# Kernel tuning notes

Measured on AMD Instinct MI355X. Metric: run time of the kernel, lower is better.

## Reference

```python
import jax, jax.numpy as jnp
import numpy as np

NEG = -1e30  # safe 'log zero' for fp32 (avoids -inf NaNs in grads)


def _ctc_loss(logits, targets, input_lengths, target_lengths):
    """PyTorch-semantics CTC loss: blank=0, reduction='mean', zero_infinity=True.
    logits: [B,T,C] (pre-log-softmax), targets: [B,S] padded, lengths: [B].
    """
    B, T, C = logits.shape
    S = targets.shape[1]
    L = 2 * S + 1  # extended target length (blanks interleaved)
    logp = jax.nn.log_softmax(logits, axis=-1)  # [B,T,C]

    # extended targets: blank, y1, blank, y2, ..., blank
    ext = jnp.zeros((B, L), jnp.int32).at[:, 1::2].set(targets.astype(jnp.int32))
    lp_ext = jnp.take_along_axis(
        logp, jnp.broadcast_to(ext[:, None, :], (B, T, L)), axis=2)  # [B,T,L]

    pos = jnp.arange(L)
    ext_m2 = jnp.pad(ext, ((0, 0), (2, 0)))[:, :L]
    can_skip = (ext != 0) & (ext != ext_m2) & (pos >= 2)  # [B,L]

    def shift(a, k):
        return jnp.pad(a, ((0, 0), (k, 0)), constant_values=NEG)[:, :L]

    def lse3(a, b, c):
        m = jnp.maximum(jnp.maximum(a, b), c)
        return m + jnp.log(jnp.exp(a - m) + jnp.exp(b - m) + jnp.exp(c - m))

    alpha0 = (jnp.full((B, L), NEG, logits.dtype)
              .at[:, 0].set(lp_ext[:, 0, 0])
              .at[:, 1].set(lp_ext[:, 0, 1]))

    def step(alpha, xs):
        lp_t, t = xs  # lp_t: [B,L]
        a2 = shift(alpha, 1)
        a3 = jnp.where(can_skip, shift(alpha, 2), NEG)
        new = lp_t + lse3(alpha, a2, a3)
        # freeze alpha once past each sample's input_length
        alpha = jnp.where((t < input_lengths)[:, None], new, alpha)
        return alpha, None

    lp_T = jnp.swapaxes(lp_ext, 0, 1)  # [T,B,L]
    alpha, _ = jax.lax.scan(step, alpha0, (lp_T[1:], jnp.arange(1, T)))

    i1 = (2 * target_lengths - 1).astype(jnp.int32)
    i2 = (2 * target_lengths).astype(jnp.int32)
    a_last = jnp.take_along_axis(alpha, i1[:, None], axis=1)[:, 0]
    a_blank = jnp.take_along_axis(alpha, i2[:, None], axis=1)[:, 0]
    loss = -jnp.logaddexp(a_last, a_blank)  # [B]
    loss = jnp.where(loss > 1e29, 0.0, loss)  # zero_infinity=True
    return jnp.mean(loss / target_lengths.astype(loss.dtype))


def setup_inputs() -> dict:
    key = jax.random.key(0)
    ks = jax.random.split(key, 8)
    B, T = 32, 2000
    C_err, S_err = 4, 50
    C_ph, S_ph = 64, 200
    error_logits = jax.random.normal(ks[0], (B, T, C_err), jnp.float32)
    phoneme_logits = jax.random.normal(ks[1], (B, T, C_ph), jnp.float32)
    # labels in [1, C): blank=0 never appears in targets
    error_targets = jax.random.randint(ks[2], (B, S_err), 1, C_err, jnp.int32)
    phoneme_targets = jax.random.randint(ks[3], (B, S_ph), 1, C_ph, jnp.int32)
    error_input_lengths = jax.random.randint(ks[4], (B,), T - T // 4, T + 1, jnp.int32)
    phoneme_input_lengths = jax.random.randint(ks[5], (B,), T - T // 4, T + 1, jnp.int32)
    error_target_lengths = jax.random.randint(ks[6], (B,), S_err // 2, S_err + 1, jnp.int32)
    phoneme_target_lengths = jax.random.randint(ks[7], (B,), S_ph // 2, S_ph + 1, jnp.int32)
    return {
        "error_logits": error_logits,
        "phoneme_logits": phoneme_logits,
        "error_targets": error_targets,
        "phoneme_targets": phoneme_targets,
        "error_input_lengths": error_input_lengths,
        "phoneme_input_lengths": phoneme_input_lengths,
        "error_target_lengths": error_target_lengths,
        "phoneme_target_lengths": phoneme_target_lengths,
    }


def reference(error_logits, phoneme_logits, error_targets, phoneme_targets,
              error_input_lengths, phoneme_input_lengths,
              error_target_lengths, phoneme_target_lengths):
    error_weight = 1.0
    phoneme_weight = 1.0
    error_loss = _ctc_loss(error_logits, error_targets,
                           error_input_lengths, error_target_lengths)
    phoneme_loss = _ctc_loss(phoneme_logits, phoneme_targets,
                             phoneme_input_lengths, phoneme_target_lengths)
    total_loss = error_weight * error_loss + phoneme_weight * phoneme_loss
    return total_loss
```

## Files before the change

kernel.cpp:

```cpp
#include <hip/hip_runtime.h>
#include <math.h>


static constexpr float  LOG2E = 1.4426950408889634f;
static constexpr double LN2D  = 0.6931471805599453;
static constexpr int GROWS = 2032;

#define DPP_WAVE_SHR1   0x138
#define DPP_ROW_SHR(n)  (0x110 | (n))
#define DPP_ROW_BCAST15 0x142
#define DPP_ROW_BCAST31 0x143

__device__ __forceinline__ float fexp2(float x) {
  return __builtin_amdgcn_exp2f(x);
}
__device__ __forceinline__ float flog2(float x) {
  return __builtin_amdgcn_logf(x);
}

__device__ __forceinline__ double dpp_shr1_f64(double x) {
  int lo = __double2loint(x), hi = __double2hiint(x);
  lo = __builtin_amdgcn_update_dpp(0, lo, DPP_WAVE_SHR1, 0xf, 0xf, true);
  hi = __builtin_amdgcn_update_dpp(0, hi, DPP_WAVE_SHR1, 0xf, 0xf, true);
  return __hiloint2double(hi, lo);
}

__device__ __forceinline__ int imax2(int a, int b) { return a > b ? a : b; }

__device__ __forceinline__ int wave_imax(int v) {
  v = imax2(v, __builtin_amdgcn_update_dpp(0, v, DPP_ROW_SHR(1), 0xf, 0xf, true));
  v = imax2(v, __builtin_amdgcn_update_dpp(0, v, DPP_ROW_SHR(2), 0xf, 0xf, true));
  v = imax2(v, __builtin_amdgcn_update_dpp(0, v, DPP_ROW_SHR(4), 0xf, 0xf, true));
  v = imax2(v, __builtin_amdgcn_update_dpp(0, v, DPP_ROW_SHR(8), 0xf, 0xf, true));
  v = imax2(v, __builtin_amdgcn_update_dpp(0, v, DPP_ROW_BCAST15, 0xf, 0xf, true));
  v = imax2(v, __builtin_amdgcn_update_dpp(0, v, DPP_ROW_BCAST31, 0xf, 0xf, true));
  return __builtin_amdgcn_readlane(v, 63);
}

__device__ __forceinline__ void wait_lgkm0() {
  __builtin_amdgcn_sched_barrier(0);
  __builtin_amdgcn_s_waitcnt(49279);
  __builtin_amdgcn_sched_barrier(0);
}


__global__ __launch_bounds__(256) void gather_ph_kernel(
    const float* __restrict__ ph_logits, const float* __restrict__ err_logits,
    const int* __restrict__ ph_tgt,
    float* __restrict__ Gph, float* __restrict__ Lpb_ph,
    float* __restrict__ Lpb_er, float* __restrict__ out) {
  const int bx = blockIdx.x, b = blockIdx.y;
  const int tid = threadIdx.x;
  const int lane = tid & 63, wv = tid >> 6;

  if (bx == 0 && b == 0 && tid == 0) *out = 0.f;

  if (wv == 0 && lane < 32) {
    const int t = bx * 32 + lane;
    if (t < 2000) {
      const float4 v = *(const float4*)(err_logits + ((size_t)b * 2000 + t) * 4);
      const float z0 = v.x * LOG2E;
      const float s = fexp2(z0) + fexp2(v.y * LOG2E) + fexp2(v.z * LOG2E) +
                      fexp2(v.w * LOG2E);
      Lpb_er[(size_t)b * GROWS + t] = z0 - flog2(s);
    }
  }

  const int* tb = ph_tgt + b * 200;
  int idx[4];
  float msk[4];
#pragma unroll
  for (int k = 0; k < 4; ++k) {
    const int si = lane * 4 + k;
    const int cls = (si < 200) ? tb[si] : 0;
    idx[k] = cls << 2;
    msk[k] = (si < 200) ? 1.0f : 0.0f;
  }
  const int t0 = (bx * 4 + wv) * 8;
  float z[8], e[8], s[8];
#pragma unroll
  for (int u = 0; u < 8; ++u) {
    const int t = t0 + u;
    const int tc = (t < 2000) ? t : 1999;
    z[u] = ph_logits[((size_t)b * 2000 + tc) * 64 + lane] * LOG2E;
    e[u] = fexp2(z[u]);
    s[u] = e[u];
  }
#pragma unroll
  for (int off = 32; off >= 1; off >>= 1) {
#pragma unroll
    for (int u = 0; u < 8; ++u) s[u] += __shfl_xor(s[u], off, 64);
  }
#pragma unroll
  for (int u = 0; u < 8; ++u) {
    const int t = t0 + u;
    if (t < 2000) {
      const float e0 = __int_as_float(
          __builtin_amdgcn_readlane(__float_as_int(e[u]), 0));
      const float inv0 = 1.0f / e0;
      float o[4];
#pragma unroll
      for (int k = 0; k < 4; ++k) {
        const float v = __int_as_float(
            __builtin_amdgcn_ds_bpermute(idx[k], __float_as_int(e[u])));
        o[k] = msk[k] * v * inv0;
      }
      *(float4*)(Gph + ((size_t)b * GROWS + t) * 256 + lane * 4) =
          make_float4(o[0], o[1], o[2], o[3]);
      if (lane == 0)
        Lpb_ph[(size_t)b * GROWS + t] = z[u] - flog2(s[u]);
    }
  }
}

template <int P> struct RowP { float v[P]; };

__device__ __forceinline__ RowP<4> ld4(const float* p) {
  RowP<4> r;
  const float4 a = *(const float4*)p;
  r.v[0] = a.x; r.v[1] = a.y; r.v[2] = a.z; r.v[3] = a.w;
  return r;
}

template <int P>
__device__ __forceinline__ void bl_renorm(double (&B)[P], double (&L)[P],
                                          int& K) {
  double mm = B[0];
#pragma unroll
  for (int k = 0; k < P; ++k) mm = fmax(fmax(mm, B[k]), L[k]);
  const int ex = (__double2hiint(mm) >> 20) & 0x7ff;
  const int emax = wave_imax(ex);
  if (emax > 0) {
    int d = 1523 - emax;
    if (d > 1023) d = 1023;
    if (d < -1022) d = -1022;
    const double sc = __hiloint2double((d + 1023) << 20, 0);
#pragma unroll
    for (int k = 0; k < P; ++k) { B[k] *= sc; L[k] *= sc; }
    K += d;
  }
}

template <int P>
__device__ __forceinline__ void bl_step(double (&B)[P], double (&L)[P],
                                        const double (&skipm)[P],
                                        const RowP<P>& f) {
  const double Lm1 = dpp_shr1_f64(L[P - 1]);
  double nB[P], nL[P];
#pragma unroll
  for (int k = 0; k < P; ++k) {
    const double Lp = (k >= 1) ? L[k - 1] : Lm1;
    nB[k] = B[k] + Lp;
    nL[k] = (double)f.v[k] * fma(skipm[k], Lp, B[k] + L[k]);
  }
#pragma unroll
  for (int k = 0; k < P; ++k) { B[k] = nB[k]; L[k] = nL[k]; }
}

__device__ __forceinline__ float spb_sum(const float* __restrict__ Lpb,
                                         int len, int lane) {
  float spb = 0.f;
  for (int t0 = lane; t0 < len; t0 += 512) {
#pragma unroll
    for (int u = 0; u < 8; ++u) {
      const int t = t0 + u * 64;
      const int tc = (t < len) ? t : 0;
      const float v = Lpb[tc];
      spb += (t < len) ? v : 0.0f;
    }
  }
#pragma unroll
  for (int off = 32; off >= 1; off >>= 1) spb += __shfl_xor(spb, off, 64);
  return spb;
}

__global__ __launch_bounds__(64) void ctc_chains2_kernel(
    const float* __restrict__ Gph, const float* __restrict__ err_logits,
    const int* __restrict__ ph_tgt, const int* __restrict__ err_tgt,
    const int* __restrict__ err_il, const int* __restrict__ ph_il,
    const int* __restrict__ err_tl, const int* __restrict__ ph_tl,
    const float* __restrict__ Lpb_ph, const float* __restrict__ Lpb_er,
    float* __restrict__ out) {
  __shared__ double sa[512];
  const int blk = blockIdx.x;
  const int lane = threadIdx.x;

  if (blk < 32) {
    constexpr int S = 50;
    const int c = blk;
    const int* tb = err_tgt + c * 50;
    int len = err_il[c]; if (len > 2000) len = 2000;
    const int tl = err_tl[c];
    const float4* zr = (const float4*)(err_logits + (size_t)c * 2000 * 4);

    const float spb = spb_sum(Lpb_er + (size_t)c * GROWS, len, lane);
    const int c1 = tb[(lane < S) ? lane : (S - 1)];
    const float fmask = (lane < S) ? 1.0f : 0.0f;
    double skipm[1];
    skipm[0] = (lane >= 1 && lane < S && tb[lane] != tb[lane - 1]) ? 1.0 : 0.0;

    double B[1], L[1];
    B[0] = 0.0; L[0] = 0.0;
    {
      const float4 q0 = zr[0];
      const int c0 = tb[0];
      const float zc = (c0 == 1) ? q0.y : (c0 == 2) ? q0.z : q0.w;
      if (lane == 0) {
        B[0] = 1.0;
        L[0] = (double)fexp2((zc - q0.x) * LOG2E);
      }
    }
    int K = 0;

    const int nsteps = len - 1;
    const int ng = nsteps / 8;
    float4 bufA[8], bufB[8];
    if (ng >= 1) {
#pragma unroll
      for (int u = 0; u < 8; ++u) bufA[u] = zr[1 + u];
    }
    if (ng >= 2) {
#pragma unroll
      for (int u = 0; u < 8; ++u) bufB[u] = zr[9 + u];
    }
    int g = 0;
    for (; g + 2 <= ng; g += 2) {
      bl_renorm<1>(B, L, K);
      {
        const int gn = (g + 2 < ng) ? (g + 2) : 0;
        const float4* nx = zr + 1 + gn * 8;
#pragma unroll
        for (int u = 0; u < 8; ++u) {
          RowP<1> f;
          const float4 q = bufA[u];
          const float zc = (c1 == 1) ? q.y : (c1 == 2) ? q.z : q.w;
          f.v[0] = fmask * fexp2((zc - q.x) * LOG2E);
          bl_step<1>(B, L, skipm, f);
          bufA[u] = nx[u];
        }
      }
      bl_renorm<1>(B, L, K);
      {
        const int gn = (g + 3 < ng) ? (g + 3) : 0;
        const float4* nx = zr + 1 + gn * 8;
#pragma unroll
        for (int u = 0; u < 8; ++u) {
          RowP<1> f;
          const float4 q = bufB[u];
          const float zc = (c1 == 1) ? q.y : (c1 == 2) ? q.z : q.w;
          f.v[0] = fmask * fexp2((zc - q.x) * LOG2E);
          bl_step<1>(B, L, skipm, f);
          bufB[u] = nx[u];
        }
      }
    }
    if (g < ng) {
      bl_renorm<1>(B, L, K);
#pragma unroll
      for (int u = 0; u < 8; ++u) {
        RowP<1> f;
        const float4 q = bufA[u];
        const float zc = (c1 == 1) ? q.y : (c1 == 2) ? q.z : q.w;
        f.v[0] = fmask * fexp2((zc - q.x) * LOG2E);
        bl_step<1>(B, L, skipm, f);
      }
      ++g;
    }
    {
      const int tstart = 1 + ng * 8;
      float4 bufT[7];
#pragma unroll
      for (int u = 0; u < 7; ++u) {
        int t = tstart + u;
        if (t > nsteps) t = (nsteps > 0) ? nsteps : 1;
        bufT[u] = zr[t];
      }
#pragma unroll
      for (int u = 0; u < 7; ++u) {
        if (tstart + u <= nsteps) {
          if (u == 0) bl_renorm<1>(B, L, K);
          RowP<1> f;
          const float4 q = bufT[u];
          const float zc = (c1 == 1) ? q.y : (c1 == 2) ? q.z : q.w;
          f.v[0] = fmask * fexp2((zc - q.x) * LOG2E);
          bl_step<1>(B, L, skipm, f);
        }
      }
    }

    double* saB = sa;
    double* saL = sa + 64;
    saB[lane] = B[0];
    saL[lane] = L[0];
    wait_lgkm0();
    if (lane == 0) {
      const double a = saL[tl - 1] + saB[tl];
      float loss = (float)((double)K * LN2D - log(a) - (double)spb * LN2D);
      if (!(loss < 1e29f)) loss = 0.f;
      atomicAdd(out, loss / ((float)tl * 32.0f));
    }
    return;
  }

  constexpr int P = 4, S = 200, LSTRIDE = 256;
  const int b = blk - 32;
  const int* tb = ph_tgt + b * 200;
  int len = ph_il[b]; if (len > 2000) len = 2000;
  const int tl = ph_tl[b];
  const float* Glab = Gph + (size_t)b * GROWS * 256;
  const float* gp = Glab + lane * P;

  const float spb = spb_sum(Lpb_ph + (size_t)b * GROWS, len, lane);

  double skipm[P];
#pragma unroll
  for (int k = 0; k < P; ++k) {
    const int s = lane * P + k;
    skipm[k] = (s >= 1 && s < S && tb[s] != tb[s - 1]) ? 1.0 : 0.0;
  }

  double B[P], L[P];
#pragma unroll
  for (int k = 0; k < P; ++k) { B[k] = 0.0; L[k] = 0.0; }
  {
    const float r0 = Glab[0];
    if (lane == 0) { B[0] = 1.0; L[0] = (double)r0; }
  }
  int K = 0;

  const int ngroups = (len - 1) / 16;

  RowP<P> bufA[16], bufB[16];
  if (ngroups >= 1) {
    const float* rb = gp + (size_t)1 * LSTRIDE;
#pragma unroll
    for (int u = 0; u < 16; ++u) bufA[u] = ld4(rb + (size_t)u * LSTRIDE);
  }
  if (ngroups >= 2) {
    const float* rb = gp + (size_t)17 * LSTRIDE;
#pragma unroll
    for (int u = 0; u < 16; ++u) bufB[u] = ld4(rb + (size_t)u * LSTRIDE);
  }

  int g = 0;
  for (; g + 2 <= ngroups; g += 2) {
    {
      bl_renorm<P>(B, L, K);
      const int gn = (g + 2 < ngroups) ? (g + 2) : 0;
      const float* nx = gp + (size_t)(1 + gn * 16) * LSTRIDE;
#pragma unroll
      for (int u = 0; u < 16; ++u) {
        bl_step<P>(B, L, skipm, bufA[u]);
        bufA[u] = ld4(nx + (size_t)u * LSTRIDE);
      }
    }
    {
      bl_renorm<P>(B, L, K);
      const int gn = (g + 3 < ngroups) ? (g + 3) : 0;
      const float* nx = gp + (size_t)(1 + gn * 16) * LSTRIDE;
#pragma unroll
      for (int u = 0; u < 16; ++u) {
        bl_step<P>(B, L, skipm, bufB[u]);
        bufB[u] = ld4(nx + (size_t)u * LSTRIDE);
      }
    }
  }
  if (g < ngroups) {
    bl_renorm<P>(B, L, K);
#pragma unroll
    for (int u = 0; u < 16; ++u) bl_step<P>(B, L, skipm, bufA[u]);
    ++g;
  }

  {
    const int tstart = 1 + ngroups * 16;
    RowP<P> bufT[15];
#pragma unroll
    for (int u = 0; u < 15; ++u) {
      int t = tstart + u;
      if (t > len - 1) t = len - 1;
      bufT[u] = ld4(gp + (size_t)t * LSTRIDE);
    }
#pragma unroll
    for (int u = 0; u < 15; ++u) {
      const int t = tstart + u;
      if (t < len) {
        if (u == 0) bl_renorm<P>(B, L, K);
        bl_step<P>(B, L, skipm, bufT[u]);
      }
    }
  }

  double* saB = sa;
  double* saL = sa + 64 * P;
#pragma unroll
  for (int k = 0; k < P; ++k) {
    saB[lane * P + k] = B[k];
    saL[lane * P + k] = L[k];
  }
  wait_lgkm0();
  if (lane == 0) {
    const double a = saL[tl - 1] + saB[tl];
    float loss = (float)((double)K * LN2D - log(a) - (double)spb * LN2D);
    if (!(loss < 1e29f)) loss = 0.f;
    atomicAdd(out, loss / ((float)tl * 32.0f));
  }
}


__global__ __launch_bounds__(256) void softmax4_kernel(
    const float* __restrict__ x, float* __restrict__ p, int nrows) {
  int r = blockIdx.x * blockDim.x + threadIdx.x;
  if (r >= nrows) return;
  float4 v = *reinterpret_cast<const float4*>(x + (size_t)r * 4);
  float z0 = v.x * LOG2E, z1 = v.y * LOG2E, z2 = v.z * LOG2E, z3 = v.w * LOG2E;
  float m = fmaxf(fmaxf(z0, z1), fmaxf(z2, z3));
  float e0 = fexp2(z0 - m), e1 = fexp2(z1 - m);
  float e2 = fexp2(z2 - m), e3 = fexp2(z3 - m);
  float inv = 1.0f / (e0 + e1 + e2 + e3);
  float4 o;
  o.x = e0 * inv; o.y = e1 * inv; o.z = e2 * inv; o.w = e3 * inv;
  *reinterpret_cast<float4*>(p + (size_t)r * 4) = o;
}

__global__ __launch_bounds__(256) void softmax64_kernel(
    const float* __restrict__ x, float* __restrict__ p, int nrows) {
  int row = blockIdx.x * 4 + (threadIdx.x >> 6);
  int lane = threadIdx.x & 63;
  if (row >= nrows) return;
  float z = x[(size_t)row * 64 + lane] * LOG2E;
  float m = z;
#pragma unroll
  for (int off = 32; off >= 1; off >>= 1) m = fmaxf(m, __shfl_xor(m, off, 64));
  float e = fexp2(z - m);
  float s = e;
#pragma unroll
  for (int off = 32; off >= 1; off >>= 1) s += __shfl_xor(s, off, 64);
  p[(size_t)row * 64 + lane] = e * (1.0f / s);
}

template <int C, int S, int R>
__device__ __forceinline__ void ctc_chain_lin_fb(
    const float* __restrict__ p_b, const int* __restrict__ tgt_b,
    int len, int tl, float* __restrict__ out, double* sa) {
  constexpr int L = 2 * S + 1;
  const int lane = threadIdx.x;
  int idx[R];
  double skipm[R];
#pragma unroll
  for (int j = 0; j < R; ++j) {
    const int l = lane * R + j;
    int cls = 0;
    bool sk = false;
    if (l & 1) {
      const int s = (l - 1) >> 1;
      const int sc = (s < S) ? s : (S - 1);
      cls = tgt_b[sc];
      if (s >= 1 && s < S) sk = (cls != tgt_b[s - 1]);
    }
    idx[j] = cls * 4;
    skipm[j] = sk ? 1.0 : 0.0;
  }
  double alpha[R];
#pragma unroll
  for (int j = 0; j < R; ++j) {
    const int l = lane * R + j;
    alpha[j] = (l <= 1) ? (double)p_b[idx[j] >> 2] : 0.0;
  }
  int K = 0;
  const int cl = lane & (C - 1);
  float rv = p_b[(size_t)((1 < len - 1) ? 1 : (len - 1)) * C + cl];
  float pf[R];
#pragma unroll
  for (int j = 0; j < R; ++j)
    pf[j] = __int_as_float(__builtin_amdgcn_ds_bpermute(idx[j], __float_as_int(rv)));
  rv = p_b[(size_t)((2 < len - 1) ? 2 : (len - 1)) * C + cl];
  for (int t = 1; t < len; ++t) {
    if ((t & 31) == 0) {
      double m = alpha[0];
#pragma unroll
      for (int j = 1; j < R; ++j) m = fmax(m, alpha[j]);
#pragma unroll
      for (int off = 1; off < 64; off <<= 1) m = fmax(m, __shfl_xor(m, off, 64));
      const long long bits = __double_as_longlong(m);
      const int e = (int)((bits >> 52) & 0x7FF);
      if (e > 0) {
        const double sc = __longlong_as_double((long long)(2046 - e) << 52);
#pragma unroll
        for (int j = 0; j < R; ++j) alpha[j] *= sc;
        K += 1023 - e;
      }
    }
    const int tn = (t + 2 < len) ? (t + 2) : (len - 1);
    const float rvn = p_b[(size_t)tn * C + cl];
    float pfn[R];
#pragma unroll
    for (int j = 0; j < R; ++j)
      pfn[j] = __int_as_float(__builtin_amdgcn_ds_bpermute(idx[j], __float_as_int(rv)));
    double am1 = __shfl_up(alpha[R - 1], 1, 64);
    double am2 = __shfl_up(alpha[R - 2], 1, 64);
    if (lane == 0) { am1 = 0.0; am2 = 0.0; }
    double na[R];
#pragma unroll
    for (int j = 0; j < R; ++j) {
      const double a0 = alpha[j];
      const double a1 = (j >= 1) ? alpha[j - 1] : am1;
      const double a2 = (j >= 2) ? alpha[j - 2] : ((j == 1) ? am1 : am2);
      double s = a0 + a1;
      s = fma(skipm[j], a2, s);
      na[j] = (double)pf[j] * s;
    }
#pragma unroll
    for (int j = 0; j < R; ++j) alpha[j] = na[j];
#pragma unroll
    for (int j = 0; j < R; ++j) pf[j] = pfn[j];
    rv = rvn;
  }
#pragma unroll
  for (int j = 0; j < R; ++j) {
    const int l = lane * R + j;
    if (l < L) sa[l] = alpha[j];
  }
  __syncthreads();
  if (lane == 0) {
    const double a = sa[2 * tl - 1] + sa[2 * tl];
    float loss = (float)((double)K * LN2D - log(a));
    if (!(loss < 1e29f)) loss = 0.0f;
    atomicAdd(out, loss / ((float)tl * 32.0f));
  }
}

__global__ __launch_bounds__(64) void ctc_chains_fb_kernel(
    const float* __restrict__ p_err, const float* __restrict__ p_ph,
    const int* __restrict__ err_tgt, const int* __restrict__ ph_tgt,
    const int* __restrict__ err_il, const int* __restrict__ ph_il,
    const int* __restrict__ err_tl, const int* __restrict__ ph_tl,
    float* __restrict__ out) {
  __shared__ double sa[512];
  const int T = 2000;
  const int blk = blockIdx.x;
  if (blk < 32) {
    const int b = blk;
    int len = err_il[b]; if (len > T) len = T;
    ctc_chain_lin_fb<4, 50, 2>(p_err + (size_t)b * T * 4, err_tgt + b * 50, len,
                               err_tl[b], out, sa);
  } else {
    const int b = blk - 32;
    int len = ph_il[b]; if (len > T) len = T;
    ctc_chain_lin_fb<64, 200, 7>(p_ph + (size_t)b * T * 64, ph_tgt + b * 200,
                                 len, ph_tl[b], out, sa);
  }
}


extern "C" void kernel_launch(void* const* d_in, const int* in_sizes, int n_in,
                              void* d_out, int out_size, void* d_ws,
                              size_t ws_size, hipStream_t stream) {
  const float* err_logits = (const float*)d_in[0];
  const float* ph_logits  = (const float*)d_in[1];
  const int* err_tgt = (const int*)d_in[2];
  const int* ph_tgt  = (const int*)d_in[3];
  const int* err_il  = (const int*)d_in[4];
  const int* ph_il   = (const int*)d_in[5];
  const int* err_tl  = (const int*)d_in[6];
  const int* ph_tl   = (const int*)d_in[7];
  float* out = (float*)d_out;

  const size_t gph = (size_t)32 * GROWS * 256;
  const size_t lpb = (size_t)32 * GROWS;
  const size_t need = (gph + 2 * lpb) * sizeof(float);

  if (ws_size >= need) {
    float* Gph = (float*)d_ws;
    float* Lpb_ph = Gph + gph;
    float* Lpb_er = Lpb_ph + lpb;
    gather_ph_kernel<<<dim3(63, 32), 256, 0, stream>>>(
        ph_logits, err_logits, ph_tgt, Gph, Lpb_ph, Lpb_er, out);
    ctc_chains2_kernel<<<64, 64, 0, stream>>>(
        Gph, err_logits, ph_tgt, err_tgt, err_il, ph_il, err_tl, ph_tl,
        Lpb_ph, Lpb_er, out);
  } else {
    (void)hipMemsetAsync(d_out, 0, sizeof(float), stream);
    const int B = 32, T = 2000;
    const int rows = B * T;
    float* p_err = (float*)d_ws;
    float* p_ph  = p_err + (size_t)rows * 4;
    softmax4_kernel<<<(rows + 255) / 256, 256, 0, stream>>>(err_logits, p_err, rows);
    softmax64_kernel<<<(rows + 3) / 4, 256, 0, stream>>>(ph_logits, p_ph, rows);
    ctc_chains_fb_kernel<<<64, 64, 0, stream>>>(p_err, p_ph, err_tgt, ph_tgt,
                                                err_il, ph_il, err_tl, ph_tl, out);
  }
}
```

Before: 201.9 us.

## Split phoneme CTC chain across two wavefronts with LDS ring handoff

The phoneme alpha recursion now runs on two wavefronts per sample instead of one. Wave 0 handles states 0-99 and wave 1 handles states 100-199, each with two states per lane instead of four. Wave 0 publishes its boundary state and scale exponent per timestep into an LDS ring with release/acquire atomics, and wave 1 trails a few steps behind, consuming those values with exponent rescaling. This shortens the serial per-step dependent chain per wave, at the cost of spin-wait synchronisation, extra LDS traffic and a more complex loss combine across differing scale factors.

```diff
diff --git a/kernel.cpp b/kernel.cpp
--- a/kernel.cpp
+++ b/kernel.cpp
@@ -115,11 +115,8 @@
 
 template <int P> struct RowP { float v[P]; };
 
-__device__ __forceinline__ RowP<4> ld4(const float* p) {
-  RowP<4> r;
-  const float4 a = *(const float4*)p;
-  r.v[0] = a.x; r.v[1] = a.y; r.v[2] = a.z; r.v[3] = a.w;
-  return r;
+__device__ __forceinline__ float2 ld2(const float* p) {
+  return *(const float2*)p;
 }
 
 template <int P>
@@ -157,6 +154,39 @@
   for (int k = 0; k < P; ++k) { B[k] = nB[k]; L[k] = nL[k]; }
 }
 
+__device__ __forceinline__ int bl_renorm2(double& B0, double& B1,
+                                          double& L0, double& L1, int& K) {
+  const double mm = fmax(fmax(B0, B1), fmax(L0, L1));
+  const int ex = (__double2hiint(mm) >> 20) & 0x7ff;
+  const int emax = wave_imax(ex);
+  if (emax > 0) {
+    int d = 1523 - emax;
+    if (d > 1023) d = 1023;
+    if (d < -1022) d = -1022;
+    const double sc = __hiloint2double((d + 1023) << 20, 0);
+    B0 *= sc; B1 *= sc; L0 *= sc; L1 *= sc;
+    K += d;
+  }
+  return emax;
+}
+
+__device__ __forceinline__ void bl_step2(double& B0, double& B1,
+                                         double& L0, double& L1,
+                                         double sk0, double sk1, float2 f,
+                                         double inj, bool hasInj, int lane) {
+  double Lm1 = dpp_shr1_f64(L1);
+  if (hasInj) Lm1 = (lane == 0) ? inj : Lm1;
+  const double Lp0 = Lm1, Lp1 = L0;
+  const double nB0 = B0 + Lp0;
+  const double nB1 = B1 + Lp1;
+  const double t0 = fma(sk0, Lp0, B0 + L0);
+  const double t1 = fma(sk1, Lp1, B1 + L1);
+  L0 = (double)f.x * t0;
+  L1 = (double)f.y * t1;
+  B0 = nB0;
+  B1 = nB1;
+}
+
 __device__ __forceinline__ float spb_sum(const float* __restrict__ Lpb,
                                          int len, int lane) {
   float spb = 0.f;
@@ -174,18 +204,23 @@
   return spb;
 }
 
-__global__ __launch_bounds__(64) void ctc_chains2_kernel(
+__global__ __launch_bounds__(128) void ctc_chains_split_kernel(
     const float* __restrict__ Gph, const float* __restrict__ err_logits,
     const int* __restrict__ ph_tgt, const int* __restrict__ err_tgt,
     const int* __restrict__ err_il, const int* __restrict__ ph_il,
     const int* __restrict__ err_tl, const int* __restrict__ ph_tl,
     const float* __restrict__ Lpb_ph, const float* __restrict__ Lpb_er,
     float* __restrict__ out) {
-  __shared__ double sa[512];
+  __shared__ double ring_v[2048];
+  __shared__ int    ring_k[2048];
+  __shared__ int    cnt;
+  __shared__ double saB[256], saL[256];
+  __shared__ int    Kw2[2];
   const int blk = blockIdx.x;
-  const int lane = threadIdx.x;
 
   if (blk < 32) {
+    if (threadIdx.x >= 64) return;
+    const int lane = threadIdx.x;
     constexpr int S = 50;
     const int c = blk;
     const int* tb = err_tgt + c * 50;
@@ -288,8 +323,6 @@
       }
     }
 
-    double* saB = sa;
-    double* saL = sa + 64;
     saB[lane] = B[0];
     saL[lane] = L[0];
     wait_lgkm0();
@@ -302,106 +335,181 @@
     return;
   }
 
-  constexpr int P = 4, S = 200, LSTRIDE = 256;
+  constexpr int S = 200, LSTRIDE = 256;
   const int b = blk - 32;
+  const int wv = threadIdx.x >> 6;
+  const int lane = threadIdx.x & 63;
   const int* tb = ph_tgt + b * 200;
   int len = ph_il[b]; if (len > 2000) len = 2000;
   const int tl = ph_tl[b];
   const float* Glab = Gph + (size_t)b * GROWS * 256;
-  const float* gp = Glab + lane * P;
-
-  const float spb = spb_sum(Lpb_ph + (size_t)b * GROWS, len, lane);
-
-  double skipm[P];
-#pragma unroll
-  for (int k = 0; k < P; ++k) {
-    const int s = lane * P + k;
-    skipm[k] = (s >= 1 && s < S && tb[s] != tb[s - 1]) ? 1.0 : 0.0;
-  }
-
-  double B[P], L[P];
-#pragma unroll
-  for (int k = 0; k < P; ++k) { B[k] = 0.0; L[k] = 0.0; }
-  {
-    const float r0 = Glab[0];
-    if (lane == 0) { B[0] = 1.0; L[0] = (double)r0; }
-  }
-  int K = 0;
-
-  const int ngroups = (len - 1) / 16;
-
-  RowP<P> bufA[16], bufB[16];
-  if (ngroups >= 1) {
-    const float* rb = gp + (size_t)1 * LSTRIDE;
-#pragma unroll
-    for (int u = 0; u < 16; ++u) bufA[u] = ld4(rb + (size_t)u * LSTRIDE);
-  }
-  if (ngroups >= 2) {
-    const float* rb = gp + (size_t)17 * LSTRIDE;
-#pragma unroll
-    for (int u = 0; u < 16; ++u) bufB[u] = ld4(rb + (size_t)u * LSTRIDE);
-  }
-
-  int g = 0;
-  for (; g + 2 <= ngroups; g += 2) {
+
+  const int cbase = wv * 100 + lane * 2;
+  const float* gp = Glab + cbase;
+  const int p0 = cbase, p1 = cbase + 1;
+  const double sk0 =
+      (p0 >= 1 && p0 < S && tb[p0] != tb[p0 - 1]) ? 1.0 : 0.0;
+  const double sk1 = (p1 < S && tb[p1] != tb[p1 - 1]) ? 1.0 : 0.0;
+
+  if (threadIdx.x == 0) { cnt = 0; ring_v[0] = 0.0; ring_k[0] = 0; }
+  __syncthreads();
+
+  const int nsteps = len - 1;
+  float spb = 0.f;
+
+  if (wv == 0) {
+    double B0 = 0.0, B1 = 0.0, L0 = 0.0, L1 = 0.0;
+    if (lane == 0) { B0 = 1.0; L0 = (double)Glab[0]; }
+    int K = 0;
+
+    const int ng = nsteps / 16;
+    float2 bufA[16], bufB[16];
+    if (ng >= 1) {
+      const float* rb = gp + (size_t)1 * LSTRIDE;
+#pragma unroll
+      for (int u = 0; u < 16; ++u) bufA[u] = ld2(rb + (size_t)u * LSTRIDE);
+    }
+    if (ng >= 2) {
+      const float* rb = gp + (size_t)17 * LSTRIDE;
+#pragma unroll
+      for (int u = 0; u < 16; ++u) bufB[u] = ld2(rb + (size_t)u * LSTRIDE);
+    }
+
+    int t = 1;
+    int g = 0;
+    for (; g + 2 <= ng; g += 2) {
+      bl_renorm2(B0, B1, L0, L1, K);
+      {
+        const int gn = (g + 2 < ng) ? (g + 2) : 0;
+        const float* nx = gp + (size_t)(1 + gn * 16) * LSTRIDE;
+#pragma unroll
+        for (int u = 0; u < 16; ++u) {
+          bl_step2(B0, B1, L0, L1, sk0, sk1, bufA[u], 0.0, false, lane);
+          if (lane == 49) {
+            ring_v[t] = L1;
+            ring_k[t] = K;
+            __hip_atomic_store(&cnt, t, __ATOMIC_RELEASE,
+                               __HIP_MEMORY_SCOPE_WORKGROUP);
+          }
+          bufA[u] = ld2(nx + (size_t)u * LSTRIDE);
+          ++t;
+        }
+      }
+      bl_renorm2(B0, B1, L0, L1, K);
+      {
+        const int gn = (g + 3 < ng) ? (g + 3) : 0;
+        const float* nx = gp + (size_t)(1 + gn * 16) * LSTRIDE;
+#pragma unroll
+        for (int u = 0; u < 16; ++u) {
+          bl_step2(B0, B1, L0, L1, sk0, sk1, bufB[u], 0.0, false, lane);
+          if (lane == 49) {
+            ring_v[t] = L1;
+            ring_k[t] = K;
+            __hip_atomic_store(&cnt, t, __ATOMIC_RELEASE,
+                               __HIP_MEMORY_SCOPE_WORKGROUP);
+          }
+          bufB[u] = ld2(nx + (size_t)u * LSTRIDE);
+          ++t;
+        }
+      }
+    }
+    if (g < ng) {
+      bl_renorm2(B0, B1, L0, L1, K);
+#pragma unroll
+      for (int u = 0; u < 16; ++u) {
+        bl_step2(B0, B1, L0, L1, sk0, sk1, bufA[u], 0.0, false, lane);
+        if (lane == 49) {
+          ring_v[t] = L1;
+          ring_k[t] = K;
+          __hip_atomic_store(&cnt, t, __ATOMIC_RELEASE,
+                             __HIP_MEMORY_SCOPE_WORKGROUP);
+        }
+        ++t;
+      }
+      ++g;
+    }
     {
-      bl_renorm<P>(B, L, K);
-      const int gn = (g + 2 < ngroups) ? (g + 2) : 0;
-      const float* nx = gp + (size_t)(1 + gn * 16) * LSTRIDE;
-#pragma unroll
-      for (int u = 0; u < 16; ++u) {
-        bl_step<P>(B, L, skipm, bufA[u]);
-        bufA[u] = ld4(nx + (size_t)u * LSTRIDE);
-      }
-    }
-    {
-      bl_renorm<P>(B, L, K);
-      const int gn = (g + 3 < ngroups) ? (g + 3) : 0;
-      const float* nx = gp + (size_t)(1 + gn * 16) * LSTRIDE;
-#pragma unroll
-      for (int u = 0; u < 16; ++u) {
-        bl_step<P>(B, L, skipm, bufB[u]);
-        bufB[u] = ld4(nx + (size_t)u * LSTRIDE);
-      }
-    }
-  }
-  if (g < ngroups) {
-    bl_renorm<P>(B, L, K);
-#pragma unroll
-    for (int u = 0; u < 16; ++u) bl_step<P>(B, L, skipm, bufA[u]);
-    ++g;
-  }
-
-  {
-    const int tstart = 1 + ngroups * 16;
-    RowP<P> bufT[15];
-#pragma unroll
-    for (int u = 0; u < 15; ++u) {
-      int t = tstart + u;
-      if (t > len - 1) t = len - 1;
-      bufT[u] = ld4(gp + (size_t)t * LSTRIDE);
-    }
-#pragma unroll
-    for (int u = 0; u < 15; ++u) {
-      const int t = tstart + u;
-      if (t < len) {
-        if (u == 0) bl_renorm<P>(B, L, K);
-        bl_step<P>(B, L, skipm, bufT[u]);
-      }
-    }
-  }
-
-  double* saB = sa;
-  double* saL = sa + 64 * P;
-#pragma unroll
-  for (int k = 0; k < P; ++k) {
-    saB[lane * P + k] = B[k];
-    saL[lane * P + k] = L[k];
-  }
-  wait_lgkm0();
-  if (lane == 0) {
-    const double a = saL[tl - 1] + saB[tl];
-    float loss = (float)((double)K * LN2D - log(a) - (double)spb * LN2D);
+      const int tstart = 1 + ng * 16;
+      float2 bufT[15];
+#pragma unroll
+      for (int u = 0; u < 15; ++u) {
+        int tt = tstart + u;
+        if (tt > nsteps) tt = (nsteps > 0) ? nsteps : 1;
+        bufT[u] = ld2(gp + (size_t)tt * LSTRIDE);
+      }
+#pragma unroll
+      for (int u = 0; u < 15; ++u) {
+        if (tstart + u <= nsteps) {
+          if (u == 0) bl_renorm2(B0, B1, L0, L1, K);
+          bl_step2(B0, B1, L0, L1, sk0, sk1, bufT[u], 0.0, false, lane);
+          if (lane == 49) {
+            ring_v[tstart + u] = L1;
+            ring_k[tstart + u] = K;
+            __hip_atomic_store(&cnt, tstart + u, __ATOMIC_RELEASE,
+                               __HIP_MEMORY_SCOPE_WORKGROUP);
+          }
+        }
+      }
+    }
+
+    spb = spb_sum(Lpb_ph + (size_t)b * GROWS, len, lane);
+
+    if (p0 < 100) { saB[p0] = B0; saL[p0] = L0; }
+    if (p1 < 100) { saB[p1] = B1; saL[p1] = L1; }
+    if (lane == 0) Kw2[0] = K;
+  } else {
+    double B0 = 0.0, B1 = 0.0, L0 = 0.0, L1 = 0.0;
+    int K = 0;
+    int t = 1;
+    while (t <= nsteps) {
+      const int tgtc = ((t + 6) < nsteps) ? (t + 6) : nsteps;
+      while (__hip_atomic_load(&cnt, __ATOMIC_ACQUIRE,
+                               __HIP_MEMORY_SCOPE_WORKGROUP) < tgtc)
+        __builtin_amdgcn_s_sleep(1);
+      double bv[8];
+      int bk[8];
+#pragma unroll
+      for (int j = 0; j < 8; ++j) {
+        bv[j] = ring_v[t - 1 + j];
+        bk[j] = ring_k[t - 1 + j];
+      }
+      const int emax = bl_renorm2(B0, B1, L0, L1, K);
+      if (emax == 0) K = bk[0];
+      float2 fr[8];
+#pragma unroll
+      for (int j = 0; j < 8; ++j) {
+        int tt = t + j;
+        if (tt > nsteps) tt = nsteps;
+        fr[j] = ld2(gp + (size_t)tt * LSTRIDE);
+      }
+#pragma unroll
+      for (int u = 0; u < 8; ++u) {
+        if (t + u <= nsteps) {
+          int d = K - bk[u];
+          if (d > 512) d = 512;
+          if (d < -1022) d = -1022;
+          const double sc = __hiloint2double((d + 1023) << 20, 0);
+          bl_step2(B0, B1, L0, L1, sk0, sk1, fr[u], bv[u] * sc, true, lane);
+        }
+      }
+      t += 8;
+    }
+    saB[p0] = B0; saL[p0] = L0;
+    saB[p1] = B1; saL[p1] = L1;
+    if (lane == 0) Kw2[1] = K;
+  }
+  __syncthreads();
+  if (threadIdx.x == 0) {
+    const int iL = tl - 1, iB = tl;
+    const int KL = (iL >= 100) ? Kw2[1] : Kw2[0];
+    const int KB = (iB >= 100) ? Kw2[1] : Kw2[0];
+    const double vL = saL[iL], vB = saB[iB];
+    const int Kref = (KL < KB) ? KL : KB;
+    int dL = Kref - KL; if (dL < -1022) dL = -1022;
+    int dB = Kref - KB; if (dB < -1022) dB = -1022;
+    const double A = vL * __hiloint2double((dL + 1023) << 20, 0) +
+                     vB * __hiloint2double((dB + 1023) << 20, 0);
+    float loss = (float)((double)Kref * LN2D - log(A) - (double)spb * LN2D);
     if (!(loss < 1e29f)) loss = 0.f;
     atomicAdd(out, loss / ((float)tl * 32.0f));
   }
@@ -576,7 +684,7 @@
     float* Lpb_er = Lpb_ph + lpb;
     gather_ph_kernel<<<dim3(63, 32), 256, 0, stream>>>(
         ph_logits, err_logits, ph_tgt, Gph, Lpb_ph, Lpb_er, out);
-    ctc_chains2_kernel<<<64, 64, 0, stream>>>(
+    ctc_chains_split_kernel<<<64, 128, 0, stream>>>(
         Gph, err_logits, ph_tgt, err_tgt, err_il, ph_il, err_tl, ph_tl,
         Lpb_ph, Lpb_er, out);
   } else {
```

Result: slower. 334.0 us (+65.5%).
